# Kernel optimization log

Measured on AMD Instinct MI355X. Metric: run time of the kernel, lower is better.

Reference implementation:

```python
import jax, jax.numpy as jnp
import numpy as np

B, N, E = 2, 2048, 1024
HQ, HKV = 16, 4           # query heads, kv heads
G = HQ // HKV             # groups (== HKV by construction; required by source einsum)
D = E // HQ               # head_dim = 64
KV_E = D * HKV            # kv projection dim = 256
LN_EPS = 1e-5


def _layernorm(x, g, b):
    mu = jnp.mean(x, axis=-1, keepdims=True)
    var = jnp.mean(jnp.square(x - mu), axis=-1, keepdims=True)
    return (x - mu) * jax.lax.rsqrt(var + LN_EPS) * g + b


def setup_inputs() -> dict:
    key = jax.random.key(0)
    ks = jax.random.split(key, 5)
    s = 0.02
    return {
        "x": jax.random.normal(ks[0], (B, N, E), dtype=jnp.float32),
        "Wq": jax.random.normal(ks[1], (E, E), dtype=jnp.float32) * s,
        "Wk": jax.random.normal(ks[2], (E, KV_E), dtype=jnp.float32) * s,
        "Wv": jax.random.normal(ks[3], (E, KV_E), dtype=jnp.float32) * s,
        "Wout": jax.random.normal(ks[4], (E, E), dtype=jnp.float32) * s,
        "ln_g": jnp.ones((E,), dtype=jnp.float32),
        "ln_b": jnp.zeros((E,), dtype=jnp.float32),
    }


def reference(x, Wq, Wk, Wv, Wout, ln_g, ln_b):
    b, n, _ = x.shape
    # projections
    q = (x @ Wq).reshape(b, n, HQ, D).transpose(0, 2, 1, 3)   # b hq n d
    k = (x @ Wk).reshape(b, n, HKV, D).transpose(0, 2, 1, 3)  # b hkv s d
    v = (x @ Wv).reshape(b, n, HKV, D).transpose(0, 2, 1, 3)  # b hkv s d
    # split query heads: (h g) with h=HKV outer, g=G inner -> b hkv g n d
    q = q.reshape(b, HKV, G, n, D)
    scale = jnp.asarray(np.sqrt(D), dtype=x.dtype)
    scores = jnp.einsum('bhgnd,bhsd->bhgns', q, k) / scale    # b hkv g n s
    causal = jnp.tril(jnp.ones((n, n), dtype=bool))           # n s
    scores = jnp.where(causal[None, None, None, :, :], scores, jnp.asarray(-jnp.inf, x.dtype))
    attn = jax.nn.softmax(scores, axis=-1)                    # b i=hkv j=g n s
    # Faithful to source's mislabeled einsum: value head axis is indexed by the
    # GROUP index j (valid because G == HKV here).
    out = jnp.einsum('bijns,bjsd->bijnd', attn, v)            # b i j n d
    # rearrange 'b g h n d -> b n (h g) d' with g=i, h=j -> merged head order (j, i)
    out = out.transpose(0, 3, 2, 1, 4).reshape(b, n, HQ * D)  # b n E
    out = _layernorm(out, ln_g, ln_b) @ Wout
    # rearrange 'b g h n s -> b n s (h g)' then mean over n
    attn_w = attn.transpose(0, 3, 4, 2, 1).reshape(b, n, n, HQ).mean(axis=1)  # b s HQ
    return (out, attn_w)
```

## Files before the change

### kernel.cpp

```cpp
#include <hip/hip_runtime.h>

#define BB 2
#define NN 2048
#define EE 1024
#define HQH 16
#define DD 64
#define KVE 256
#define QKVW 1536

typedef short bf16x8 __attribute__((ext_vector_type(8)));
typedef float f32x4 __attribute__((ext_vector_type(4)));
typedef unsigned short u16;
typedef unsigned int u32;

#if __has_builtin(__builtin_amdgcn_exp2f)
#define EXP2(x) __builtin_amdgcn_exp2f(x)
#else
#define EXP2(x) exp2f(x)
#endif

#define QSCALE 0.18033688011112042f

__device__ __forceinline__ u16 f2bf(float f) {
    unsigned u = __float_as_uint(f);
    u += 0x7FFFu + ((u >> 16) & 1u);
    return (u16)(u >> 16);
}
__device__ __forceinline__ float bf2f(u16 h) {
    return __uint_as_float(((unsigned)h) << 16);
}

#define GLOAD_LDS16(gp, lp) __builtin_amdgcn_global_load_lds( \
    (const __attribute__((address_space(1))) unsigned int*)(gp), \
    (__attribute__((address_space(3))) unsigned int*)(lp), 16, 0, 0)

__device__ __forceinline__ bf16x8 xpose8(bf16x8 v, int q) {
    union { bf16x8 v; u32 r[4]; } u_;
    u_.v = v;
    u32 r0 = u_.r[0], r1 = u_.r[1], r2 = u_.r[2], r3 = u_.r[3];
    u32 x, y, t0;
    x = (q & 4) ? r0 : r2;  y = (q & 4) ? r1 : r3;
    x = __shfl_xor(x, 4);   y = __shfl_xor(y, 4);
    if (q & 4) { r0 = x; r1 = y; } else { r2 = x; r3 = y; }
    x = (q & 2) ? r0 : r1;  y = (q & 2) ? r2 : r3;
    x = __shfl_xor(x, 2);   y = __shfl_xor(y, 2);
    if (q & 2) { r0 = x; r2 = y; } else { r1 = x; r3 = y; }
    t0 = __shfl_xor(r0, 1); r0 = (q & 1) ? ((t0 >> 16) | (r0 & 0xFFFF0000u)) : ((r0 & 0xFFFFu) | (t0 << 16));
    t0 = __shfl_xor(r1, 1); r1 = (q & 1) ? ((t0 >> 16) | (r1 & 0xFFFF0000u)) : ((r1 & 0xFFFFu) | (t0 << 16));
    t0 = __shfl_xor(r2, 1); r2 = (q & 1) ? ((t0 >> 16) | (r2 & 0xFFFF0000u)) : ((r2 & 0xFFFFu) | (t0 << 16));
    t0 = __shfl_xor(r3, 1); r3 = (q & 1) ? ((t0 >> 16) | (r3 & 0xFFFF0000u)) : ((r3 & 0xFFFFu) | (t0 << 16));
    u_.r[0] = r0; u_.r[1] = r1; u_.r[2] = r2; u_.r[3] = r3;
    return u_.v;
}

__global__ __launch_bounds__(256)
void conv_bf16(const float* __restrict__ in, u16* __restrict__ out) {
    int i = (blockIdx.x * 256 + threadIdx.x) * 8;
    float4 a = *(const float4*)&in[i];
    float4 b = *(const float4*)&in[i + 4];
    bf16x8 p;
    p[0] = f2bf(a.x); p[1] = f2bf(a.y); p[2] = f2bf(a.z); p[3] = f2bf(a.w);
    p[4] = f2bf(b.x); p[5] = f2bf(b.y); p[6] = f2bf(b.z); p[7] = f2bf(b.w);
    *(bf16x8*)&out[i] = p;
}

__global__ __launch_bounds__(256)
void transp_bf16(const float* __restrict__ W, u16* __restrict__ WT, int Nc) {
    __shared__ float tile[32][33];
    int k0 = blockIdx.x * 32, n0 = blockIdx.y * 32;
    int tx = threadIdx.x & 31, ty = threadIdx.x >> 5;
#pragma unroll
    for (int i = 0; i < 4; ++i)
        tile[ty + i * 8][tx] = W[(size_t)(k0 + ty + i * 8) * Nc + n0 + tx];
    __syncthreads();
#pragma unroll
    for (int i = 0; i < 4; ++i)
        WT[(size_t)(n0 + ty + i * 8) * EE + k0 + tx] = f2bf(tile[tx][ty + i * 8]);
}

__global__ __launch_bounds__(256)
void gemm_mfma(const u16* __restrict__ A, const u16* __restrict__ BT,
               void* __restrict__ C, int K, int ldc, int obf16,
               float qscale, int nq) {
    __shared__ __attribute__((aligned(16))) u16 sA[128 * 64];
    __shared__ __attribute__((aligned(16))) u16 sB[128 * 64];
    int t = threadIdx.x;
    int lane = t & 63, w = t >> 6;
    int wr = w >> 1, wc = w & 1;
    int l15 = lane & 15, lg = lane >> 4;
    int m0 = blockIdx.y * 128, n0 = blockIdx.x * 128;

    f32x4 acc[4][4];
#pragma unroll
    for (int mi = 0; mi < 4; ++mi)
#pragma unroll
        for (int ni = 0; ni < 4; ++ni) acc[mi][ni] = (f32x4){0.f, 0.f, 0.f, 0.f};

    int srow = lane >> 3;
    int schunk = (lane & 7) ^ srow;
    const u16* ga = A + (size_t)(m0 + w * 32 + srow) * K + schunk * 8;
    const u16* gb = BT + (size_t)(n0 + w * 32 + srow) * K + schunk * 8;
    char* lA = (char*)sA + w * 4096;
    char* lB = (char*)sB + w * 4096;

    for (int k0 = 0; k0 < K; k0 += 64) {
#pragma unroll
        for (int i = 0; i < 4; ++i) {
            GLOAD_LDS16(ga + (size_t)i * 8 * K + k0, lA + i * 1024);
            GLOAD_LDS16(gb + (size_t)i * 8 * K + k0, lB + i * 1024);
        }
        __syncthreads();
#pragma unroll
        for (int ks = 0; ks < 2; ++ks) {
            bf16x8 af[4], bfr[4];
#pragma unroll
            for (int mi = 0; mi < 4; ++mi) {
                int row = wr * 64 + mi * 16 + l15;
                af[mi] = *(const bf16x8*)((char*)sA +
                    ((row * 128 + lg * 16 + ks * 64) ^ ((row & 7) << 4)));
            }
#pragma unroll
            for (int ni = 0; ni < 4; ++ni) {
                int row = wc * 64 + ni * 16 + l15;
                bfr[ni] = *(const bf16x8*)((char*)sB +
                    ((row * 128 + lg * 16 + ks * 64) ^ ((row & 7) << 4)));
            }
#pragma unroll
            for (int mi = 0; mi < 4; ++mi)
#pragma unroll
                for (int ni = 0; ni < 4; ++ni)
                    acc[mi][ni] = __builtin_amdgcn_mfma_f32_16x16x32_bf16(
                        af[mi], bfr[ni], acc[mi][ni], 0, 0, 0);
        }
        __syncthreads();
    }

#pragma unroll
    for (int mi = 0; mi < 4; ++mi) {
        int rbase = m0 + wr * 64 + mi * 16 + lg * 4;
#pragma unroll
        for (int ni = 0; ni < 4; ++ni) {
            int col = n0 + wc * 64 + ni * 16 + l15;
            float sc = (col < nq) ? qscale : 1.0f;
            if (obf16) {
                u16* Cb = (u16*)C;
#pragma unroll
                for (int r = 0; r < 4; ++r)
                    Cb[(size_t)(rbase + r) * ldc + col] = f2bf(acc[mi][ni][r] * sc);
            } else {
                float* Cf = (float*)C;
#pragma unroll
                for (int r = 0; r < 4; ++r)
                    Cf[(size_t)(rbase + r) * ldc + col] = acc[mi][ni][r] * sc;
            }
        }
    }
}

__global__ __launch_bounds__(256)
void flash_attn(const u16* __restrict__ QKV, u16* __restrict__ AOb,
                float* __restrict__ mbuf, float* __restrict__ lbuf) {
    __shared__ __attribute__((aligned(16))) u16 sK[64 * 64];
    __shared__ __attribute__((aligned(16))) u16 sV[64 * 64];
    __shared__ __attribute__((aligned(16))) u16 sP[4 * 16 * 64];

    int blk = blockIdx.x;
    int pk = blk & 7;
    int bh = blk >> 3;
    int hq = bh & 15;
    int b = bh >> 4;
    int ih = hq >> 2, jh = hq & 3;
    int hm = jh * 4 + ih;
    int t = threadIdx.x;
    int lane = t & 63, w = t >> 6;
    int l15 = lane & 15, lg = lane >> 4;
    int q8 = t & 7;

    const u16* Kg = QKV + (size_t)b * NN * QKVW + EE + ih * DD;
    const u16* Vg = QKV + (size_t)b * NN * QKVW + EE + KVE + jh * DD;
    char* pbase = (char*)sP + w * 2048;

    for (int half = 0; half < 2; ++half) {
        int ntile = half ? (15 - pk) : pk;
        int n0 = ntile * 128;

        bf16x8 qf[2][2];
#pragma unroll
        for (int tt = 0; tt < 2; ++tt)
#pragma unroll
            for (int h = 0; h < 2; ++h)
                qf[tt][h] = *(const bf16x8*)(QKV +
                    (size_t)(b * NN + n0 + w * 32 + tt * 16 + l15) * QKVW + hq * DD + lg * 8 + h * 32);

        f32x4 o[2][4];
        float mrow[2][4], lrow[2][4];
#pragma unroll
        for (int tt = 0; tt < 2; ++tt)
#pragma unroll
            for (int i = 0; i < 4; ++i) {
                o[tt][i] = (f32x4){0.f, 0.f, 0.f, 0.f};
                mrow[tt][i] = -1e30f;
                lrow[tt][i] = 0.f;
            }

        int send = n0 + 128;
        bf16x8 kreg[2], vreg[2];
#pragma unroll
        for (int it = 0; it < 2; ++it) {
            int lin = t + it * 256;
            kreg[it] = *(const bf16x8*)(Kg + (size_t)(lin >> 3) * QKVW + (lin & 7) * 8);
            vreg[it] = *(const bf16x8*)(Vg + (size_t)((lin >> 6) * 8 + q8) * QKVW + ((lin >> 3) & 7) * 8);
        }

        for (int s0 = 0; s0 < send; s0 += 64) {
#pragma unroll
            for (int it = 0; it < 2; ++it) {
                int lin = t + it * 256;
                int sk = lin >> 3, c8k = (lin & 7) * 8;
                *(bf16x8*)((char*)sK + ((sk * 128 + c8k * 2) ^ ((sk & 7) << 4))) = kreg[it];
                bf16x8 vt = xpose8(vreg[it], q8);
                int d = ((lin >> 3) & 7) * 8 + q8;
                int sbase = (lin >> 6) * 8;
                *(bf16x8*)((char*)sV + ((d * 128 + sbase * 2) ^ (q8 << 4))) = vt;
            }
            if (s0 + 64 < send) {
#pragma unroll
                for (int it = 0; it < 2; ++it) {
                    int lin = t + it * 256;
                    kreg[it] = *(const bf16x8*)(Kg + (size_t)(s0 + 64 + (lin >> 3)) * QKVW + (lin & 7) * 8);
                    vreg[it] = *(const bf16x8*)(Vg + (size_t)(s0 + 64 + (lin >> 6) * 8 + q8) * QKVW + ((lin >> 3) & 7) * 8);
                }
            }
            __syncthreads();

            f32x4 sf[2][4];
#pragma unroll
            for (int sub = 0; sub < 4; ++sub) {
                int row = sub * 16 + l15;
                int swz = (row & 7) << 4;
                bf16x8 k0 = *(const bf16x8*)((char*)sK + ((row * 128 + lg * 16) ^ swz));
                bf16x8 k1 = *(const bf16x8*)((char*)sK + ((row * 128 + lg * 16 + 64) ^ swz));
#pragma unroll
                for (int tt = 0; tt < 2; ++tt) {
                    f32x4 z = {0.f, 0.f, 0.f, 0.f};
                    z = __builtin_amdgcn_mfma_f32_16x16x32_bf16(qf[tt][0], k0, z, 0, 0, 0);
                    sf[tt][sub] = __builtin_amdgcn_mfma_f32_16x16x32_bf16(qf[tt][1], k1, z, 0, 0, 0);
                }
            }

#pragma unroll
            for (int tt = 0; tt < 2; ++tt) {
                int nb_min = n0 + w * 32 + tt * 16;
                int nbase = nb_min + lg * 4;
                float mcur[4] = {-1e30f, -1e30f, -1e30f, -1e30f};
                if (s0 + 63 > nb_min) {
#pragma unroll
                    for (int sub = 0; sub < 4; ++sub) {
                        int sg = s0 + sub * 16 + l15;
#pragma unroll
                        for (int r = 0; r < 4; ++r) {
                            float sc = sf[tt][sub][r];
                            sc = (sg <= nbase + r) ? sc : -1e30f;
                            sf[tt][sub][r] = sc;
                            mcur[r] = fmaxf(mcur[r], sc);
                        }
                    }
                } else {
#pragma unroll
                    for (int sub = 0; sub < 4; ++sub)
#pragma unroll
                        for (int r = 0; r < 4; ++r)
                            mcur[r] = fmaxf(mcur[r], sf[tt][sub][r]);
                }
#pragma unroll
                for (int r = 0; r < 4; ++r) {
                    mcur[r] = fmaxf(mcur[r], __shfl_xor(mcur[r], 1));
                    mcur[r] = fmaxf(mcur[r], __shfl_xor(mcur[r], 2));
                    mcur[r] = fmaxf(mcur[r], __shfl_xor(mcur[r], 4));
                    mcur[r] = fmaxf(mcur[r], __shfl_xor(mcur[r], 8));
                }
                float alpha[4], rs[4];
#pragma unroll
                for (int r = 0; r < 4; ++r) {
                    float mnew = fmaxf(mrow[tt][r], mcur[r]);
                    alpha[r] = EXP2(mrow[tt][r] - mnew);
                    mrow[tt][r] = mnew;
                    rs[r] = 0.f;
                }
#pragma unroll
                for (int sub = 0; sub < 4; ++sub)
#pragma unroll
                    for (int r = 0; r < 4; ++r) {
                        float p = EXP2(sf[tt][sub][r] - mrow[tt][r]);
                        sf[tt][sub][r] = p;
                        rs[r] += p;
                    }
#pragma unroll
                for (int r = 0; r < 4; ++r) {
                    rs[r] += __shfl_xor(rs[r], 1);
                    rs[r] += __shfl_xor(rs[r], 2);
                    rs[r] += __shfl_xor(rs[r], 4);
                    rs[r] += __shfl_xor(rs[r], 8);
                    lrow[tt][r] = lrow[tt][r] * alpha[r] + rs[r];
                }
#pragma unroll
                for (int sd = 0; sd < 4; ++sd)
#pragma unroll
                    for (int r = 0; r < 4; ++r) o[tt][sd][r] *= alpha[r];

#pragma unroll
                for (int sub = 0; sub < 4; ++sub)
#pragma unroll
                    for (int r = 0; r < 4; ++r) {
                        int rr = lg * 4 + r;
                        int col = sub * 16 + l15;
                        *(u16*)(pbase + ((rr * 128 + col * 2) ^ ((rr & 7) << 4))) =
                            f2bf(sf[tt][sub][r]);
                    }
                int pswz = (l15 & 7) << 4;
                bf16x8 pa0 = *(const bf16x8*)(pbase + ((l15 * 128 + lg * 16) ^ pswz));
                bf16x8 pa1 = *(const bf16x8*)(pbase + ((l15 * 128 + lg * 16 + 64) ^ pswz));
#pragma unroll
                for (int sd = 0; sd < 4; ++sd) {
                    int dr = sd * 16 + l15;
                    int vswz = (dr & 7) << 4;
                    bf16x8 v0 = *(const bf16x8*)((char*)sV + ((dr * 128 + lg * 16) ^ vswz));
                    bf16x8 v1 = *(const bf16x8*)((char*)sV + ((dr * 128 + lg * 16 + 64) ^ vswz));
                    o[tt][sd] = __builtin_amdgcn_mfma_f32_16x16x32_bf16(pa0, v0, o[tt][sd], 0, 0, 0);
                    o[tt][sd] = __builtin_amdgcn_mfma_f32_16x16x32_bf16(pa1, v1, o[tt][sd], 0, 0, 0);
                }
            }
            __syncthreads();
        }

#pragma unroll
        for (int tt = 0; tt < 2; ++tt) {
            float inv[4];
#pragma unroll
            for (int r = 0; r < 4; ++r) inv[r] = 1.f / lrow[tt][r];
#pragma unroll
            for (int sd = 0; sd < 4; ++sd)
#pragma unroll
                for (int r = 0; r < 4; ++r) {
                    int n = n0 + w * 32 + tt * 16 + lg * 4 + r;
                    AOb[(size_t)(b * NN + n) * EE + hm * DD + sd * 16 + l15] =
                        f2bf(o[tt][sd][r] * inv[r]);
                }
            if (l15 == 0) {
#pragma unroll
                for (int r = 0; r < 4; ++r) {
                    int n = n0 + w * 32 + tt * 16 + lg * 4 + r;
                    mbuf[(size_t)bh * NN + n] = mrow[tt][r];
                    lbuf[(size_t)bh * NN + n] = inv[r];
                }
            }
        }
    }
}

__global__ __launch_bounds__(256)
void colsum_mfma(const u16* __restrict__ QKV,
                 const float* __restrict__ mbuf, const float* __restrict__ lbuf,
                 float* __restrict__ AW) {
    int blk = blockIdx.x;
    int pk = blk & 7;
    int bh = blk >> 3;
    int hq = bh & 15;
    int b = bh >> 4;
    int ih = hq >> 2, jh = hq & 3;
    int hm = jh * 4 + ih;
    int t = threadIdx.x;
    int lane = t & 63, w = t >> 6;
    int l15 = lane & 15, lg = lane >> 4;

    for (int half = 0; half < 2; ++half) {
        int stile = half ? (15 - pk) : pk;
        int sb = stile * 128 + w * 32;

        bf16x8 kf[2][2];
#pragma unroll
        for (int st = 0; st < 2; ++st)
#pragma unroll
            for (int h = 0; h < 2; ++h)
                kf[st][h] = *(const bf16x8*)(QKV +
                    (size_t)(b * NN + sb + st * 16 + l15) * QKVW + EE + ih * DD + lg * 8 + h * 32);

        float acc[2][4] = {};
        int nstart = stile * 128;

        const u16* qp0 = QKV + (size_t)(b * NN + nstart + l15) * QKVW + hq * DD + lg * 8;
        bf16x8 q0 = *(const bf16x8*)qp0;
        bf16x8 q1 = *(const bf16x8*)(qp0 + 32);
        float mv = mbuf[(size_t)bh * NN + nstart + l15];
        float li = lbuf[(size_t)bh * NN + nstart + l15];

        for (int nn0 = nstart; nn0 < NN; nn0 += 16) {
            bf16x8 cq0 = q0, cq1 = q1;
            float cmv = mv, cli = li;
            if (nn0 + 16 < NN) {
                const u16* qp = QKV + (size_t)(b * NN + nn0 + 16 + l15) * QKVW + hq * DD + lg * 8;
                q0 = *(const bf16x8*)qp;
                q1 = *(const bf16x8*)(qp + 32);
                mv = mbuf[(size_t)bh * NN + nn0 + 16 + l15];
                li = lbuf[(size_t)bh * NN + nn0 + 16 + l15];
            }
            int n = nn0 + l15;
#pragma unroll
            for (int st = 0; st < 2; ++st) {
                f32x4 z = {0.f, 0.f, 0.f, 0.f};
                z = __builtin_amdgcn_mfma_f32_16x16x32_bf16(kf[st][0], cq0, z, 0, 0, 0);
                z = __builtin_amdgcn_mfma_f32_16x16x32_bf16(kf[st][1], cq1, z, 0, 0, 0);
#pragma unroll
                for (int r = 0; r < 4; ++r) {
                    int s = sb + st * 16 + lg * 4 + r;
                    float val = EXP2(z[r] - cmv) * cli;
                    acc[st][r] += (n >= s) ? val : 0.f;
                }
            }
        }
#pragma unroll
        for (int st = 0; st < 2; ++st)
#pragma unroll
            for (int r = 0; r < 4; ++r) {
                float a = acc[st][r];
                a += __shfl_xor(a, 1);
                a += __shfl_xor(a, 2);
                a += __shfl_xor(a, 4);
                a += __shfl_xor(a, 8);
                if (l15 == 0) {
                    int s = sb + st * 16 + lg * 4 + r;
                    AW[((size_t)b * NN + s) * HQH + hm] = a * (1.0f / NN);
                }
            }
    }
}

__global__ __launch_bounds__(256)
void layernorm_bf16(u16* __restrict__ X, const float* __restrict__ g,
                    const float* __restrict__ bt) {
    __shared__ float red[256];
    int row = blockIdx.x;
    int t = threadIdx.x;
    u16* xp = X + (size_t)row * EE;
    ushort4 v = *(ushort4*)&xp[t * 4];
    float x0 = bf2f(v.x), x1 = bf2f(v.y), x2 = bf2f(v.z), x3 = bf2f(v.w);
    red[t] = x0 + x1 + x2 + x3;
    __syncthreads();
    for (int off = 128; off > 0; off >>= 1) {
        if (t < off) red[t] += red[t + off];
        __syncthreads();
    }
    float mu = red[0] * (1.f / EE);
    __syncthreads();
    float d0 = x0 - mu, d1 = x1 - mu, d2 = x2 - mu, d3 = x3 - mu;
    red[t] = d0 * d0 + d1 * d1 + d2 * d2 + d3 * d3;
    __syncthreads();
    for (int off = 128; off > 0; off >>= 1) {
        if (t < off) red[t] += red[t + off];
        __syncthreads();
    }
    float rstd = rsqrtf(red[0] * (1.f / EE) + 1e-5f);
    float4 gg = *(const float4*)&g[t * 4];
    float4 bb = *(const float4*)&bt[t * 4];
    ushort4 o;
    o.x = f2bf(d0 * rstd * gg.x + bb.x);
    o.y = f2bf(d1 * rstd * gg.y + bb.y);
    o.z = f2bf(d2 * rstd * gg.z + bb.z);
    o.w = f2bf(d3 * rstd * gg.w + bb.w);
    *(ushort4*)&xp[t * 4] = o;
}

extern "C" void kernel_launch(void* const* d_in, const int* in_sizes, int n_in,
                              void* d_out, int out_size, void* d_ws, size_t ws_size,
                              hipStream_t stream) {
    const float* x    = (const float*)d_in[0];
    const float* Wq   = (const float*)d_in[1];
    const float* Wk   = (const float*)d_in[2];
    const float* Wv   = (const float*)d_in[3];
    const float* Wout = (const float*)d_in[4];
    const float* lng  = (const float*)d_in[5];
    const float* lnb  = (const float*)d_in[6];

    float* out = (float*)d_out;
    float* aw  = out + (size_t)BB * NN * EE;

    u16* Xb    = (u16*)d_ws;
    u16* QKVb  = Xb + (size_t)BB * NN * EE;
    u16* WqkvT = QKVb + (size_t)BB * NN * QKVW;
    u16* WoutT = WqkvT + (size_t)QKVW * EE;
    u16* AOb   = WoutT + (size_t)EE * EE;
    float* mb  = (float*)(AOb + (size_t)BB * NN * EE);
    float* lb  = mb + (size_t)BB * HQH * NN;

    dim3 blk(256);

    conv_bf16<<<BB * NN * EE / 2048, blk, 0, stream>>>(x, Xb);
    transp_bf16<<<dim3(32, 32), blk, 0, stream>>>(Wq, WqkvT, EE);
    transp_bf16<<<dim3(32, 8), blk, 0, stream>>>(Wk, WqkvT + (size_t)EE * EE, KVE);
    transp_bf16<<<dim3(32, 8), blk, 0, stream>>>(Wv, WqkvT + (size_t)(EE + KVE) * EE, KVE);
    transp_bf16<<<dim3(32, 32), blk, 0, stream>>>(Wout, WoutT, EE);

    gemm_mfma<<<dim3(QKVW / 128, BB * NN / 128), blk, 0, stream>>>(
        Xb, WqkvT, QKVb, EE, QKVW, 1, QSCALE, EE);

    int pblocks = BB * HQH * 8;
    flash_attn<<<pblocks, blk, 0, stream>>>(QKVb, AOb, mb, lb);
    colsum_mfma<<<pblocks, blk, 0, stream>>>(QKVb, mb, lb, aw);

    layernorm_bf16<<<BB * NN, blk, 0, stream>>>(AOb, lng, lnb);

    gemm_mfma<<<dim3(EE / 128, BB * NN / 128), blk, 0, stream>>>(
        AOb, WoutT, out, EE, EE, 0, 1.0f, 0);
}
```

Before: 315.8 us.

## Restructure flash attention with transposed scores, register P, double-buffered V

The flash attention kernel now computes S^T so that each lane owns one query row. P is then packed to bf16 in registers and fed straight into the PV MFMA, with no round trip through shared memory. K fragments are read directly from global memory, V is double-buffered in LDS with a single barrier per tile, and the rescale is skipped lazily when the new max rises by at most 8. Both attention kernels now launch one block per 128-row tile, twice as many blocks as before, in place of the old paired-tile scheme. This trades the old balanced tile pairing for more parallelism. It also leans on the L2 cache for K reads and relies on the lazy-rescale threshold staying numerically safe.

```diff
diff --git a/kernel.cpp b/kernel.cpp
--- a/kernel.cpp
+++ b/kernel.cpp
@@ -9,6 +9,7 @@
 #define QKVW 1536
 
 typedef short bf16x8 __attribute__((ext_vector_type(8)));
+typedef short bf16x4 __attribute__((ext_vector_type(4)));
 typedef float f32x4 __attribute__((ext_vector_type(4)));
 typedef unsigned short u16;
 typedef unsigned int u32;
@@ -28,6 +29,11 @@
 }
 __device__ __forceinline__ float bf2f(u16 h) {
     return __uint_as_float(((unsigned)h) << 16);
+}
+__device__ __forceinline__ u32 cvtpk(float a, float b) {
+    u32 r;
+    asm("v_cvt_pk_bf16_f32 %0, %1, %2" : "=v"(r) : "v"(a), "v"(b));
+    return r;
 }
 
 #define GLOAD_LDS16(gp, lp) __builtin_amdgcn_global_load_lds( \
@@ -160,13 +166,213 @@
 __global__ __launch_bounds__(256)
 void flash_attn(const u16* __restrict__ QKV, u16* __restrict__ AOb,
                 float* __restrict__ mbuf, float* __restrict__ lbuf) {
-    __shared__ __attribute__((aligned(16))) u16 sK[64 * 64];
-    __shared__ __attribute__((aligned(16))) u16 sV[64 * 64];
-    __shared__ __attribute__((aligned(16))) u16 sP[4 * 16 * 64];
+    __shared__ __attribute__((aligned(16))) u16 sV[2][64 * 64];
 
     int blk = blockIdx.x;
-    int pk = blk & 7;
-    int bh = blk >> 3;
+    int ntile = 15 - (blk & 15);
+    int bh = blk >> 4;
+    int hq = bh & 15;
+    int b = bh >> 4;
+    int ih = hq >> 2, jh = hq & 3;
+    int hm = jh * 4 + ih;
+    int n0 = ntile * 128;
+    int t = threadIdx.x;
+    int lane = t & 63, w = t >> 6;
+    int l15 = lane & 15, lg = lane >> 4;
+    int q8 = t & 7;
+
+    const u16* Kg = QKV + (size_t)b * NN * QKVW + EE + ih * DD;
+    const u16* Vg = QKV + (size_t)b * NN * QKVW + EE + KVE + jh * DD;
+
+    bf16x8 qf[2][2];
+#pragma unroll
+    for (int tt = 0; tt < 2; ++tt)
+#pragma unroll
+        for (int h = 0; h < 2; ++h)
+            qf[tt][h] = *(const bf16x8*)(QKV +
+                (size_t)(b * NN + n0 + w * 32 + tt * 16 + l15) * QKVW + hq * DD + lg * 8 + h * 32);
+
+    f32x4 o[2][4];
+    float mrow[2] = {-1e30f, -1e30f};
+    float lrow[2] = {0.f, 0.f};
+#pragma unroll
+    for (int tt = 0; tt < 2; ++tt)
+#pragma unroll
+        for (int i = 0; i < 4; ++i) o[tt][i] = (f32x4){0.f, 0.f, 0.f, 0.f};
+
+    int nt = (n0 + 128) >> 6;
+    bf16x8 vr[2];
+#pragma unroll
+    for (int it = 0; it < 2; ++it) {
+        int lin = t + it * 256;
+        vr[it] = *(const bf16x8*)(Vg + (size_t)((lin >> 6) * 8 + q8) * QKVW + ((lin >> 3) & 7) * 8);
+    }
+#pragma unroll
+    for (int it = 0; it < 2; ++it) {
+        int lin = t + it * 256;
+        int d = ((lin >> 3) & 7) * 8 + q8;
+        int sbase = (lin >> 6) * 8;
+        bf16x8 vt = xpose8(vr[it], q8);
+        *(bf16x8*)((char*)sV[0] + ((d * 128 + sbase * 2) ^ (q8 << 4))) = vt;
+    }
+
+    for (int ti = 0; ti < nt; ++ti) {
+        int s0 = ti << 6;
+        if (ti + 1 < nt) {
+#pragma unroll
+            for (int it = 0; it < 2; ++it) {
+                int lin = t + it * 256;
+                vr[it] = *(const bf16x8*)(Vg +
+                    (size_t)(s0 + 64 + (lin >> 6) * 8 + q8) * QKVW + ((lin >> 3) & 7) * 8);
+            }
+        }
+        __syncthreads();
+        const char* vb = (const char*)sV[ti & 1];
+
+        f32x4 sf[2][4];
+#pragma unroll
+        for (int sub = 0; sub < 4; ++sub) {
+            const u16* kp = Kg + (size_t)(s0 + sub * 16 + l15) * QKVW + lg * 8;
+            bf16x8 k0 = *(const bf16x8*)kp;
+            bf16x8 k1 = *(const bf16x8*)(kp + 32);
+#pragma unroll
+            for (int tt = 0; tt < 2; ++tt) {
+                f32x4 z = {0.f, 0.f, 0.f, 0.f};
+                z = __builtin_amdgcn_mfma_f32_16x16x32_bf16(k0, qf[tt][0], z, 0, 0, 0);
+                sf[tt][sub] = __builtin_amdgcn_mfma_f32_16x16x32_bf16(k1, qf[tt][1], z, 0, 0, 0);
+            }
+        }
+
+        bf16x8 vf[4][2];
+#pragma unroll
+        for (int sd = 0; sd < 4; ++sd) {
+            int d = sd * 16 + l15;
+            int swz = (d & 7) << 4;
+#pragma unroll
+            for (int f = 0; f < 2; ++f) {
+                int aA = (d * 128 + (f * 32 + lg * 4) * 2) ^ swz;
+                int aB = (d * 128 + (f * 32 + 16 + lg * 4) * 2) ^ swz;
+                bf16x4 lo = *(const bf16x4*)(vb + aA);
+                bf16x4 hi = *(const bf16x4*)(vb + aB);
+                bf16x8 vv;
+                vv[0] = lo[0]; vv[1] = lo[1]; vv[2] = lo[2]; vv[3] = lo[3];
+                vv[4] = hi[0]; vv[5] = hi[1]; vv[6] = hi[2]; vv[7] = hi[3];
+                vf[sd][f] = vv;
+            }
+        }
+
+#pragma unroll
+        for (int tt = 0; tt < 2; ++tt) {
+            int ng_min = n0 + w * 32 + tt * 16;
+            int ng = ng_min + l15;
+            float mcur = -1e30f;
+            if (s0 + 63 > ng_min) {
+#pragma unroll
+                for (int sub = 0; sub < 4; ++sub)
+#pragma unroll
+                    for (int r = 0; r < 4; ++r) {
+                        int sg = s0 + sub * 16 + lg * 4 + r;
+                        float sc = (sg <= ng) ? sf[tt][sub][r] : -1e30f;
+                        sf[tt][sub][r] = sc;
+                        mcur = fmaxf(mcur, sc);
+                    }
+            } else {
+#pragma unroll
+                for (int sub = 0; sub < 4; ++sub)
+#pragma unroll
+                    for (int r = 0; r < 4; ++r) mcur = fmaxf(mcur, sf[tt][sub][r]);
+            }
+            mcur = fmaxf(mcur, __shfl_xor(mcur, 16));
+            mcur = fmaxf(mcur, __shfl_xor(mcur, 32));
+
+            float mn = mrow[tt];
+            if (!__all(mcur <= mn + 8.0f)) {
+                mn = fmaxf(mn, mcur);
+                float alpha = EXP2(mrow[tt] - mn);
+                mrow[tt] = mn;
+                lrow[tt] *= alpha;
+                float a0 = __shfl(alpha, lg * 4 + 0);
+                float a1 = __shfl(alpha, lg * 4 + 1);
+                float a2 = __shfl(alpha, lg * 4 + 2);
+                float a3 = __shfl(alpha, lg * 4 + 3);
+#pragma unroll
+                for (int sd = 0; sd < 4; ++sd) {
+                    o[tt][sd][0] *= a0; o[tt][sd][1] *= a1;
+                    o[tt][sd][2] *= a2; o[tt][sd][3] *= a3;
+                }
+            }
+            float rs = 0.f;
+#pragma unroll
+            for (int sub = 0; sub < 4; ++sub)
+#pragma unroll
+                for (int r = 0; r < 4; ++r) {
+                    float p = EXP2(sf[tt][sub][r] - mn);
+                    sf[tt][sub][r] = p;
+                    rs += p;
+                }
+            rs += __shfl_xor(rs, 16);
+            rs += __shfl_xor(rs, 32);
+            lrow[tt] += rs;
+
+            union { u32 r[4]; bf16x8 v; } pa0, pa1;
+            pa0.r[0] = cvtpk(sf[tt][0][0], sf[tt][0][1]);
+            pa0.r[1] = cvtpk(sf[tt][0][2], sf[tt][0][3]);
+            pa0.r[2] = cvtpk(sf[tt][1][0], sf[tt][1][1]);
+            pa0.r[3] = cvtpk(sf[tt][1][2], sf[tt][1][3]);
+            pa1.r[0] = cvtpk(sf[tt][2][0], sf[tt][2][1]);
+            pa1.r[1] = cvtpk(sf[tt][2][2], sf[tt][2][3]);
+            pa1.r[2] = cvtpk(sf[tt][3][0], sf[tt][3][1]);
+            pa1.r[3] = cvtpk(sf[tt][3][2], sf[tt][3][3]);
+#pragma unroll
+            for (int sd = 0; sd < 4; ++sd) {
+                o[tt][sd] = __builtin_amdgcn_mfma_f32_16x16x32_bf16(pa0.v, vf[sd][0], o[tt][sd], 0, 0, 0);
+                o[tt][sd] = __builtin_amdgcn_mfma_f32_16x16x32_bf16(pa1.v, vf[sd][1], o[tt][sd], 0, 0, 0);
+            }
+        }
+
+        if (ti + 1 < nt) {
+#pragma unroll
+            for (int it = 0; it < 2; ++it) {
+                int lin = t + it * 256;
+                int d = ((lin >> 3) & 7) * 8 + q8;
+                int sbase = (lin >> 6) * 8;
+                bf16x8 vt = xpose8(vr[it], q8);
+                *(bf16x8*)((char*)sV[(ti + 1) & 1] + ((d * 128 + sbase * 2) ^ (q8 << 4))) = vt;
+            }
+        }
+    }
+
+#pragma unroll
+    for (int tt = 0; tt < 2; ++tt) {
+        float linv = 1.f / lrow[tt];
+        if (lg == 0) {
+            int n = n0 + w * 32 + tt * 16 + l15;
+            mbuf[(size_t)bh * NN + n] = mrow[tt];
+            lbuf[(size_t)bh * NN + n] = linv;
+        }
+        float i0 = __shfl(linv, lg * 4 + 0);
+        float i1 = __shfl(linv, lg * 4 + 1);
+        float i2 = __shfl(linv, lg * 4 + 2);
+        float i3 = __shfl(linv, lg * 4 + 3);
+#pragma unroll
+        for (int sd = 0; sd < 4; ++sd) {
+            int nb = n0 + w * 32 + tt * 16 + lg * 4;
+            size_t base = (size_t)(b * NN + nb) * EE + hm * DD + sd * 16 + l15;
+            AOb[base]          = f2bf(o[tt][sd][0] * i0);
+            AOb[base + EE]     = f2bf(o[tt][sd][1] * i1);
+            AOb[base + 2 * EE] = f2bf(o[tt][sd][2] * i2);
+            AOb[base + 3 * EE] = f2bf(o[tt][sd][3] * i3);
+        }
+    }
+}
+
+__global__ __launch_bounds__(256)
+void colsum_mfma(const u16* __restrict__ QKV,
+                 const float* __restrict__ mbuf, const float* __restrict__ lbuf,
+                 float* __restrict__ AW) {
+    int blk = blockIdx.x;
+    int stile = blk & 15;
+    int bh = blk >> 4;
     int hq = bh & 15;
     int b = bh >> 4;
     int ih = hq >> 2, jh = hq & 3;
@@ -174,265 +380,63 @@
     int t = threadIdx.x;
     int lane = t & 63, w = t >> 6;
     int l15 = lane & 15, lg = lane >> 4;
-    int q8 = t & 7;
-
-    const u16* Kg = QKV + (size_t)b * NN * QKVW + EE + ih * DD;
-    const u16* Vg = QKV + (size_t)b * NN * QKVW + EE + KVE + jh * DD;
-    char* pbase = (char*)sP + w * 2048;
-
-    for (int half = 0; half < 2; ++half) {
-        int ntile = half ? (15 - pk) : pk;
-        int n0 = ntile * 128;
-
-        bf16x8 qf[2][2];
-#pragma unroll
-        for (int tt = 0; tt < 2; ++tt)
-#pragma unroll
-            for (int h = 0; h < 2; ++h)
-                qf[tt][h] = *(const bf16x8*)(QKV +
-                    (size_t)(b * NN + n0 + w * 32 + tt * 16 + l15) * QKVW + hq * DD + lg * 8 + h * 32);
-
-        f32x4 o[2][4];
-        float mrow[2][4], lrow[2][4];
-#pragma unroll
-        for (int tt = 0; tt < 2; ++tt)
-#pragma unroll
-            for (int i = 0; i < 4; ++i) {
-                o[tt][i] = (f32x4){0.f, 0.f, 0.f, 0.f};
-                mrow[tt][i] = -1e30f;
-                lrow[tt][i] = 0.f;
-            }
-
-        int send = n0 + 128;
-        bf16x8 kreg[2], vreg[2];
-#pragma unroll
-        for (int it = 0; it < 2; ++it) {
-            int lin = t + it * 256;
-            kreg[it] = *(const bf16x8*)(Kg + (size_t)(lin >> 3) * QKVW + (lin & 7) * 8);
-            vreg[it] = *(const bf16x8*)(Vg + (size_t)((lin >> 6) * 8 + q8) * QKVW + ((lin >> 3) & 7) * 8);
-        }
-
-        for (int s0 = 0; s0 < send; s0 += 64) {
-#pragma unroll
-            for (int it = 0; it < 2; ++it) {
-                int lin = t + it * 256;
-                int sk = lin >> 3, c8k = (lin & 7) * 8;
-                *(bf16x8*)((char*)sK + ((sk * 128 + c8k * 2) ^ ((sk & 7) << 4))) = kreg[it];
-                bf16x8 vt = xpose8(vreg[it], q8);
-                int d = ((lin >> 3) & 7) * 8 + q8;
-                int sbase = (lin >> 6) * 8;
-                *(bf16x8*)((char*)sV + ((d * 128 + sbase * 2) ^ (q8 << 4))) = vt;
-            }
-            if (s0 + 64 < send) {
-#pragma unroll
-                for (int it = 0; it < 2; ++it) {
-                    int lin = t + it * 256;
-                    kreg[it] = *(const bf16x8*)(Kg + (size_t)(s0 + 64 + (lin >> 3)) * QKVW + (lin & 7) * 8);
-                    vreg[it] = *(const bf16x8*)(Vg + (size_t)(s0 + 64 + (lin >> 6) * 8 + q8) * QKVW + ((lin >> 3) & 7) * 8);
-                }
-            }
-            __syncthreads();
-
-            f32x4 sf[2][4];
-#pragma unroll
-            for (int sub = 0; sub < 4; ++sub) {
-                int row = sub * 16 + l15;
-                int swz = (row & 7) << 4;
-                bf16x8 k0 = *(const bf16x8*)((char*)sK + ((row * 128 + lg * 16) ^ swz));
-                bf16x8 k1 = *(const bf16x8*)((char*)sK + ((row * 128 + lg * 16 + 64) ^ swz));
-#pragma unroll
-                for (int tt = 0; tt < 2; ++tt) {
-                    f32x4 z = {0.f, 0.f, 0.f, 0.f};
-                    z = __builtin_amdgcn_mfma_f32_16x16x32_bf16(qf[tt][0], k0, z, 0, 0, 0);
-                    sf[tt][sub] = __builtin_amdgcn_mfma_f32_16x16x32_bf16(qf[tt][1], k1, z, 0, 0, 0);
-                }
-            }
-
-#pragma unroll
-            for (int tt = 0; tt < 2; ++tt) {
-                int nb_min = n0 + w * 32 + tt * 16;
-                int nbase = nb_min + lg * 4;
-                float mcur[4] = {-1e30f, -1e30f, -1e30f, -1e30f};
-                if (s0 + 63 > nb_min) {
-#pragma unroll
-                    for (int sub = 0; sub < 4; ++sub) {
-                        int sg = s0 + sub * 16 + l15;
-#pragma unroll
-                        for (int r = 0; r < 4; ++r) {
-                            float sc = sf[tt][sub][r];
-                            sc = (sg <= nbase + r) ? sc : -1e30f;
-                            sf[tt][sub][r] = sc;
-                            mcur[r] = fmaxf(mcur[r], sc);
-                        }
-                    }
-                } else {
-#pragma unroll
-                    for (int sub = 0; sub < 4; ++sub)
-#pragma unroll
-                        for (int r = 0; r < 4; ++r)
-                            mcur[r] = fmaxf(mcur[r], sf[tt][sub][r]);
-                }
-#pragma unroll
-                for (int r = 0; r < 4; ++r) {
-                    mcur[r] = fmaxf(mcur[r], __shfl_xor(mcur[r], 1));
-                    mcur[r] = fmaxf(mcur[r], __shfl_xor(mcur[r], 2));
-                    mcur[r] = fmaxf(mcur[r], __shfl_xor(mcur[r], 4));
-                    mcur[r] = fmaxf(mcur[r], __shfl_xor(mcur[r], 8));
-                }
-                float alpha[4], rs[4];
-#pragma unroll
-                for (int r = 0; r < 4; ++r) {
-                    float mnew = fmaxf(mrow[tt][r], mcur[r]);
-                    alpha[r] = EXP2(mrow[tt][r] - mnew);
-                    mrow[tt][r] = mnew;
-                    rs[r] = 0.f;
-                }
-#pragma unroll
-                for (int sub = 0; sub < 4; ++sub)
-#pragma unroll
-                    for (int r = 0; r < 4; ++r) {
-                        float p = EXP2(sf[tt][sub][r] - mrow[tt][r]);
-                        sf[tt][sub][r] = p;
-                        rs[r] += p;
-                    }
-#pragma unroll
-                for (int r = 0; r < 4; ++r) {
-                    rs[r] += __shfl_xor(rs[r], 1);
-                    rs[r] += __shfl_xor(rs[r], 2);
-                    rs[r] += __shfl_xor(rs[r], 4);
-                    rs[r] += __shfl_xor(rs[r], 8);
-                    lrow[tt][r] = lrow[tt][r] * alpha[r] + rs[r];
-                }
-#pragma unroll
-                for (int sd = 0; sd < 4; ++sd)
-#pragma unroll
-                    for (int r = 0; r < 4; ++r) o[tt][sd][r] *= alpha[r];
-
-#pragma unroll
-                for (int sub = 0; sub < 4; ++sub)
-#pragma unroll
-                    for (int r = 0; r < 4; ++r) {
-                        int rr = lg * 4 + r;
-                        int col = sub * 16 + l15;
-                        *(u16*)(pbase + ((rr * 128 + col * 2) ^ ((rr & 7) << 4))) =
-                            f2bf(sf[tt][sub][r]);
-                    }
-                int pswz = (l15 & 7) << 4;
-                bf16x8 pa0 = *(const bf16x8*)(pbase + ((l15 * 128 + lg * 16) ^ pswz));
-                bf16x8 pa1 = *(const bf16x8*)(pbase + ((l15 * 128 + lg * 16 + 64) ^ pswz));
-#pragma unroll
-                for (int sd = 0; sd < 4; ++sd) {
-                    int dr = sd * 16 + l15;
-                    int vswz = (dr & 7) << 4;
-                    bf16x8 v0 = *(const bf16x8*)((char*)sV + ((dr * 128 + lg * 16) ^ vswz));
-                    bf16x8 v1 = *(const bf16x8*)((char*)sV + ((dr * 128 + lg * 16 + 64) ^ vswz));
-                    o[tt][sd] = __builtin_amdgcn_mfma_f32_16x16x32_bf16(pa0, v0, o[tt][sd], 0, 0, 0);
-                    o[tt][sd] = __builtin_amdgcn_mfma_f32_16x16x32_bf16(pa1, v1, o[tt][sd], 0, 0, 0);
-                }
-            }
-            __syncthreads();
-        }
-
-#pragma unroll
-        for (int tt = 0; tt < 2; ++tt) {
-            float inv[4];
-#pragma unroll
-            for (int r = 0; r < 4; ++r) inv[r] = 1.f / lrow[tt][r];
-#pragma unroll
-            for (int sd = 0; sd < 4; ++sd)
-#pragma unroll
-                for (int r = 0; r < 4; ++r) {
-                    int n = n0 + w * 32 + tt * 16 + lg * 4 + r;
-                    AOb[(size_t)(b * NN + n) * EE + hm * DD + sd * 16 + l15] =
-                        f2bf(o[tt][sd][r] * inv[r]);
-                }
+    int sb = stile * 128 + w * 32;
+
+    bf16x8 kf[2][2];
+#pragma unroll
+    for (int st = 0; st < 2; ++st)
+#pragma unroll
+        for (int h = 0; h < 2; ++h)
+            kf[st][h] = *(const bf16x8*)(QKV +
+                (size_t)(b * NN + sb + st * 16 + l15) * QKVW + EE + ih * DD + lg * 8 + h * 32);
+
+    float acc[2][4] = {};
+    int nstart = stile * 128;
+
+    const u16* qp0 = QKV + (size_t)(b * NN + nstart + l15) * QKVW + hq * DD + lg * 8;
+    bf16x8 q0 = *(const bf16x8*)qp0;
+    bf16x8 q1 = *(const bf16x8*)(qp0 + 32);
+    float mv = mbuf[(size_t)bh * NN + nstart + l15];
+    float li = lbuf[(size_t)bh * NN + nstart + l15];
+
+    for (int nn0 = nstart; nn0 < NN; nn0 += 16) {
+        bf16x8 cq0 = q0, cq1 = q1;
+        float cmv = mv, cli = li;
+        if (nn0 + 16 < NN) {
+            const u16* qp = QKV + (size_t)(b * NN + nn0 + 16 + l15) * QKVW + hq * DD + lg * 8;
+            q0 = *(const bf16x8*)qp;
+            q1 = *(const bf16x8*)(qp + 32);
+            mv = mbuf[(size_t)bh * NN + nn0 + 16 + l15];
+            li = lbuf[(size_t)bh * NN + nn0 + 16 + l15];
+        }
+        int n = nn0 + l15;
+#pragma unroll
+        for (int st = 0; st < 2; ++st) {
+            f32x4 z = {0.f, 0.f, 0.f, 0.f};
+            z = __builtin_amdgcn_mfma_f32_16x16x32_bf16(kf[st][0], cq0, z, 0, 0, 0);
+            z = __builtin_amdgcn_mfma_f32_16x16x32_bf16(kf[st][1], cq1, z, 0, 0, 0);
+#pragma unroll
+            for (int r = 0; r < 4; ++r) {
+                int s = sb + st * 16 + lg * 4 + r;
+                float val = EXP2(z[r] - cmv) * cli;
+                acc[st][r] += (n >= s) ? val : 0.f;
+            }
+        }
+    }
+#pragma unroll
+    for (int st = 0; st < 2; ++st)
+#pragma unroll
+        for (int r = 0; r < 4; ++r) {
+            float a = acc[st][r];
+            a += __shfl_xor(a, 1);
+            a += __shfl_xor(a, 2);
+            a += __shfl_xor(a, 4);
+            a += __shfl_xor(a, 8);
             if (l15 == 0) {
-#pragma unroll
-                for (int r = 0; r < 4; ++r) {
-                    int n = n0 + w * 32 + tt * 16 + lg * 4 + r;
-                    mbuf[(size_t)bh * NN + n] = mrow[tt][r];
-                    lbuf[(size_t)bh * NN + n] = inv[r];
-                }
-            }
-        }
-    }
-}
-
-__global__ __launch_bounds__(256)
-void colsum_mfma(const u16* __restrict__ QKV,
-                 const float* __restrict__ mbuf, const float* __restrict__ lbuf,
-                 float* __restrict__ AW) {
-    int blk = blockIdx.x;
-    int pk = blk & 7;
-    int bh = blk >> 3;
-    int hq = bh & 15;
-    int b = bh >> 4;
-    int ih = hq >> 2, jh = hq & 3;
-    int hm = jh * 4 + ih;
-    int t = threadIdx.x;
-    int lane = t & 63, w = t >> 6;
-    int l15 = lane & 15, lg = lane >> 4;
-
-    for (int half = 0; half < 2; ++half) {
-        int stile = half ? (15 - pk) : pk;
-        int sb = stile * 128 + w * 32;
-
-        bf16x8 kf[2][2];
-#pragma unroll
-        for (int st = 0; st < 2; ++st)
-#pragma unroll
-            for (int h = 0; h < 2; ++h)
-                kf[st][h] = *(const bf16x8*)(QKV +
-                    (size_t)(b * NN + sb + st * 16 + l15) * QKVW + EE + ih * DD + lg * 8 + h * 32);
-
-        float acc[2][4] = {};
-        int nstart = stile * 128;
-
-        const u16* qp0 = QKV + (size_t)(b * NN + nstart + l15) * QKVW + hq * DD + lg * 8;
-        bf16x8 q0 = *(const bf16x8*)qp0;
-        bf16x8 q1 = *(const bf16x8*)(qp0 + 32);
-        float mv = mbuf[(size_t)bh * NN + nstart + l15];
-        float li = lbuf[(size_t)bh * NN + nstart + l15];
-
-        for (int nn0 = nstart; nn0 < NN; nn0 += 16) {
-            bf16x8 cq0 = q0, cq1 = q1;
-            float cmv = mv, cli = li;
-            if (nn0 + 16 < NN) {
-                const u16* qp = QKV + (size_t)(b * NN + nn0 + 16 + l15) * QKVW + hq * DD + lg * 8;
-                q0 = *(const bf16x8*)qp;
-                q1 = *(const bf16x8*)(qp + 32);
-                mv = mbuf[(size_t)bh * NN + nn0 + 16 + l15];
-                li = lbuf[(size_t)bh * NN + nn0 + 16 + l15];
-            }
-            int n = nn0 + l15;
-#pragma unroll
-            for (int st = 0; st < 2; ++st) {
-                f32x4 z = {0.f, 0.f, 0.f, 0.f};
-                z = __builtin_amdgcn_mfma_f32_16x16x32_bf16(kf[st][0], cq0, z, 0, 0, 0);
-                z = __builtin_amdgcn_mfma_f32_16x16x32_bf16(kf[st][1], cq1, z, 0, 0, 0);
-#pragma unroll
-                for (int r = 0; r < 4; ++r) {
-                    int s = sb + st * 16 + lg * 4 + r;
-                    float val = EXP2(z[r] - cmv) * cli;
-                    acc[st][r] += (n >= s) ? val : 0.f;
-                }
-            }
-        }
-#pragma unroll
-        for (int st = 0; st < 2; ++st)
-#pragma unroll
-            for (int r = 0; r < 4; ++r) {
-                float a = acc[st][r];
-                a += __shfl_xor(a, 1);
-                a += __shfl_xor(a, 2);
-                a += __shfl_xor(a, 4);
-                a += __shfl_xor(a, 8);
-                if (l15 == 0) {
-                    int s = sb + st * 16 + lg * 4 + r;
-                    AW[((size_t)b * NN + s) * HQH + hm] = a * (1.0f / NN);
-                }
-            }
-    }
+                int s = sb + st * 16 + lg * 4 + r;
+                AW[((size_t)b * NN + s) * HQH + hm] = a * (1.0f / NN);
+            }
+        }
 }
 
 __global__ __launch_bounds__(256)
@@ -503,9 +507,9 @@
     gemm_mfma<<<dim3(QKVW / 128, BB * NN / 128), blk, 0, stream>>>(
         Xb, WqkvT, QKVb, EE, QKVW, 1, QSCALE, EE);
 
-    int pblocks = BB * HQH * 8;
-    flash_attn<<<pblocks, blk, 0, stream>>>(QKVb, AOb, mb, lb);
-    colsum_mfma<<<pblocks, blk, 0, stream>>>(QKVb, mb, lb, aw);
+    int ablocks = BB * HQH * 16;
+    flash_attn<<<ablocks, blk, 0, stream>>>(QKVb, AOb, mb, lb);
+    colsum_mfma<<<ablocks, blk, 0, stream>>>(QKVb, mb, lb, aw);
 
     layernorm_bf16<<<BB * NN, blk, 0, stream>>>(AOb, lng, lnb);
 
```

Result: faster. 298.0 us (-5.6%).
